# Optimization experiments

Measured on AMD Instinct MI355X. Metric: run time of the kernel, lower is better.

The kernel has to match this reference:

```python
import jax, jax.numpy as jnp
import numpy as np

# mamba-130m dims (n_layers reduced to 4 for single-device tractability)
B, L, D, DI, N, R, K, V, NL = 2, 512, 768, 1536, 16, 48, 4, 50280, 4


def setup_inputs() -> dict:
    key = jax.random.key(0)
    ks = jax.random.split(key, 10)
    s = 0.02
    return {
        "question_ids": jax.random.randint(ks[0], (B, L), 0, V, dtype=jnp.int32),
        "question_mask": jnp.ones((B, L), dtype=jnp.int32),
        "answer_ids": jax.random.randint(ks[1], (B, L), 0, V, dtype=jnp.int32),
        "answer_mask": jnp.ones((B, L), dtype=jnp.int32),
        "embed": jax.random.normal(ks[2], (V, D), jnp.float32) * s,
        "in_proj_w": jax.random.normal(ks[3], (NL, D, 2 * DI), jnp.float32) * s,
        "conv_w": jax.random.normal(ks[4], (NL, DI, K), jnp.float32) * s,
        "conv_b": jnp.zeros((NL, DI), jnp.float32),
        "x_proj_w": jax.random.normal(ks[5], (NL, DI, R + 2 * N), jnp.float32) * s,
        "dt_proj_w": jax.random.normal(ks[6], (NL, R, DI), jnp.float32) * s,
        # bias ~ -4.6 so softplus(dt) ~ 0.01, like mamba's dt init range
        "dt_proj_b": jnp.full((NL, DI), -4.6, jnp.float32),
        "A_log": jnp.broadcast_to(jnp.log(jnp.arange(1, N + 1, dtype=jnp.float32)), (NL, DI, N)) + jnp.zeros((NL, DI, N), jnp.float32),
        "D_param": jnp.ones((NL, DI), jnp.float32),
        "out_proj_w": jax.random.normal(ks[7], (NL, DI, D), jnp.float32) * s,
        "norm_w": jnp.ones((NL, D), jnp.float32),
        "norm_f_w": jnp.ones((D,), jnp.float32),
    }


def _rms(x, w, eps=1e-5):
    return x * jax.lax.rsqrt(jnp.mean(x * x, axis=-1, keepdims=True) + eps) * w


def _selective_scan(dA, dBu, Ct):
    # dA, dBu: (B, L, DI, N); Ct: (B, L, N)
    def step(h, xs):
        a, b = xs
        h = a * h + b
        return h, h

    h0 = jnp.zeros((dA.shape[0], dA.shape[2], dA.shape[3]), dA.dtype)  # (B, DI, N)
    _, hs = jax.lax.scan(step, h0, (jnp.swapaxes(dA, 0, 1), jnp.swapaxes(dBu, 0, 1)))
    hs = jnp.swapaxes(hs, 0, 1)  # (B, L, DI, N)
    return jnp.einsum('bldn,bln->bld', hs, Ct)


def _block(x, p):
    ipw, cw, cb, xpw, dtw, dtb, Alog, Dp, opw, nw = p
    h = _rms(x, nw)
    xz = h @ ipw                      # (B, L, 2*DI)
    u, z = xz[..., :DI], xz[..., DI:]
    # depthwise causal conv, kernel K
    up = jnp.pad(u, ((0, 0), (K - 1, 0), (0, 0)))
    uc = sum(up[:, k:k + u.shape[1], :] * cw[:, k] for k in range(K)) + cb
    uc = jax.nn.silu(uc)
    proj = uc @ xpw                   # (B, L, R+2N)
    dt = jax.nn.softplus(proj[..., :R] @ dtw + dtb)
    Bt = proj[..., R:R + N]
    Ct = proj[..., R + N:]
    A = -jnp.exp(Alog)                # (DI, N)
    dA = jnp.exp(dt[..., None] * A)   # (B, L, DI, N)
    dBu = (dt * uc)[..., None] * Bt[:, :, None, :]
    y = _selective_scan(dA, dBu, Ct) + uc * Dp
    y = y * jax.nn.silu(z)
    return x + y @ opw


def _lm_loss(ids, mask, embed, layers, norm_f_w):
    x = embed[ids] * mask[..., None].astype(embed.dtype)
    for p in layers:
        x = _block(x, p)
    x = _rms(x, norm_f_w)
    logits = x @ embed.T              # tied lm head, (B, L, V)
    logp = jax.nn.log_softmax(logits[:, :-1], axis=-1)
    lbl = ids[:, 1:]
    nll = -jnp.take_along_axis(logp, lbl[..., None], axis=-1)[..., 0]
    m = mask[:, 1:].astype(logp.dtype)
    return jnp.sum(nll * m) / jnp.maximum(jnp.sum(m), 1.0)


def reference(question_ids, question_mask, answer_ids, answer_mask, embed, in_proj_w, conv_w, conv_b, x_proj_w, dt_proj_w, dt_proj_b, A_log, D_param, out_proj_w, norm_w, norm_f_w):
    layers = [
        (in_proj_w[l], conv_w[l], conv_b[l], x_proj_w[l], dt_proj_w[l], dt_proj_b[l], A_log[l], D_param[l], out_proj_w[l], norm_w[l])
        for l in range(NL)
    ]
    loss_q = _lm_loss(question_ids, question_mask, embed, layers, norm_f_w)
    loss_a = _lm_loss(answer_ids, answer_mask, embed, layers, norm_f_w)
    return loss_a + loss_q
```

## Files before the change

### kernel.cpp

```cpp
#include <hip/hip_runtime.h>
#include <hip/hip_bf16.h>
#include <cstdint>
#include <cstddef>

#define T_TOK   2048
#define DM      768
#define DI      1536
#define NST     16
#define RRANK   48
#define KCONV   4
#define VOCAB   50280
#define NLAYER  4
#define SEQL    512
#define NTILE_V 393
#define NCHUNK  8
#define CHL     64

typedef __bf16 bf16x8 __attribute__((ext_vector_type(8)));
typedef float  f32x4  __attribute__((ext_vector_type(4)));

__device__ inline unsigned short f2b(float f) {
  union { float f; unsigned u; } v; v.f = f;
  unsigned r = v.u + 0x7FFFu + ((v.u >> 16) & 1u);
  return (unsigned short)(r >> 16);
}
__device__ inline float b2f(unsigned short h) {
  union { unsigned u; float f; } v; v.u = ((unsigned)h) << 16;
  return v.f;
}

__device__ inline void gload_lds16(const unsigned short* g, unsigned short* l) {
  __builtin_amdgcn_global_load_lds(
      (const __attribute__((address_space(1))) void*)g,
      (__attribute__((address_space(3))) void*)l, 16, 0, 0);
}

__global__ __launch_bounds__(256) void transpose_conv_kernel(
    const float* __restrict__ src, unsigned short* __restrict__ dst,
    int R, int C, int Rpad) {
  __shared__ float tile[32][33];
  const float* s = src + (size_t)blockIdx.z * R * C;
  unsigned short* d = dst + (size_t)blockIdx.z * C * Rpad;
  int c0 = blockIdx.x * 32, r0 = blockIdx.y * 32;
  int tx = threadIdx.x & 31, ty = threadIdx.x >> 5;
  #pragma unroll
  for (int i = 0; i < 32; i += 8) {
    int r = r0 + ty + i, c = c0 + tx;
    tile[ty + i][tx] = (r < R && c < C) ? s[(size_t)r * C + c] : 0.f;
  }
  __syncthreads();
  #pragma unroll
  for (int i = 0; i < 32; i += 8) {
    int c = c0 + ty + i, r = r0 + tx;
    if (c < C && r < Rpad) d[(size_t)c * Rpad + r] = f2b(tile[tx][ty + i]);
  }
}

__global__ __launch_bounds__(256) void cvt_embed_kernel(
    const float* __restrict__ e, unsigned short* __restrict__ eb) {
  const int n4 = VOCAB * DM / 4;
  for (int i = blockIdx.x * 256 + threadIdx.x; i < n4; i += gridDim.x * 256) {
    float4 f = *(const float4*)(e + (size_t)i * 4);
    union { unsigned long long u; unsigned short h[4]; } pk;
    pk.h[0] = f2b(f.x); pk.h[1] = f2b(f.y); pk.h[2] = f2b(f.z); pk.h[3] = f2b(f.w);
    *(unsigned long long*)(eb + (size_t)i * 4) = pk.u;
  }
}

__global__ __launch_bounds__(256) void gather_kernel(
    const int* __restrict__ qids, const int* __restrict__ qmask,
    const int* __restrict__ aids, const int* __restrict__ amask,
    const float* __restrict__ embed, float* __restrict__ x) {
  int idx = blockIdx.x * 256 + threadIdx.x;
  int t = idx / DM, d = idx - t * DM;
  int seq = t >> 9, pos = t & 511;
  const int* ids = (seq < 2) ? qids : aids;
  const int* msk = (seq < 2) ? qmask : amask;
  int s2 = seq & 1;
  int id = ids[s2 * SEQL + pos];
  float m = (float)msk[s2 * SEQL + pos];
  x[idx] = embed[(size_t)id * DM + d] * m;
}

__global__ __launch_bounds__(256) void rmsnorm_kernel(
    const float* __restrict__ x, const float* __restrict__ w,
    unsigned short* __restrict__ h) {
  int t = blockIdx.x;
  const float* xr = x + (size_t)t * DM;
  float ss = 0.f;
  for (int d = threadIdx.x; d < DM; d += 256) { float v = xr[d]; ss += v * v; }
  for (int o = 1; o < 64; o <<= 1) ss += __shfl_xor(ss, o);
  __shared__ float wsum[4];
  if ((threadIdx.x & 63) == 0) wsum[threadIdx.x >> 6] = ss;
  __syncthreads();
  ss = wsum[0] + wsum[1] + wsum[2] + wsum[3];
  float sc = rsqrtf(ss / (float)DM + 1e-5f);
  for (int d = threadIdx.x; d < DM; d += 256)
    h[(size_t)t * DM + d] = f2b(xr[d] * sc * w[d]);
}

__global__ __launch_bounds__(256) void resid_rms_kernel(
    float* __restrict__ x, const float* __restrict__ part,
    const float* __restrict__ w, unsigned short* __restrict__ h) {
  int t = blockIdx.x;
  float v[3];
  float ss = 0.f;
  #pragma unroll
  for (int j = 0; j < 3; ++j) {
    int d = threadIdx.x + j * 256;
    size_t o = (size_t)t * DM + d;
    float xv = x[o] + part[o] + part[(size_t)T_TOK * DM + o] +
               part[(size_t)2 * T_TOK * DM + o] + part[(size_t)3 * T_TOK * DM + o];
    x[o] = xv; v[j] = xv; ss += xv * xv;
  }
  for (int o = 1; o < 64; o <<= 1) ss += __shfl_xor(ss, o);
  __shared__ float wsum[4];
  if ((threadIdx.x & 63) == 0) wsum[threadIdx.x >> 6] = ss;
  __syncthreads();
  ss = wsum[0] + wsum[1] + wsum[2] + wsum[3];
  float sc = rsqrtf(ss / (float)DM + 1e-5f);
  #pragma unroll
  for (int j = 0; j < 3; ++j) {
    int d = threadIdx.x + j * 256;
    h[(size_t)t * DM + d] = f2b(v[j] * sc * w[d]);
  }
}

template <int EPI>
__global__ __launch_bounds__(256) void gemm_bf16_kernel(
    const unsigned short* __restrict__ A, int lda,
    const unsigned short* __restrict__ B, int ldb,
    float* __restrict__ C, unsigned short* __restrict__ Cbf,
    float* __restrict__ CT, int ldc,
    const float* __restrict__ bias,
    int M, int N, int K, int mtiles) {
  __shared__ __attribute__((aligned(16))) unsigned short As[2][128 * 64];
  __shared__ __attribute__((aligned(16))) unsigned short Bs[2][128 * 64];
  int bid = blockIdx.x;
  int m0 = (bid % mtiles) * 128;
  int rest = bid / mtiles;
  int n0, split = 0;
  int ntil = (N + 127) >> 7;
  if (EPI == 6) { split = rest / ntil; n0 = (rest % ntil) * 128; }
  else n0 = rest * 128;
  const unsigned short* Ap = (EPI == 6) ? A + (size_t)split * K : A;
  const unsigned short* Bp = (EPI == 6) ? B + (size_t)split * K : B;
  int tid = threadIdx.x;
  int lane = tid & 63, w = tid >> 6;
  int wr = w >> 1, wc = w & 1;
  f32x4 acc[4][4] = {};

  int lrow = lane >> 3;
  int lcol = (((lane & 7) ^ (lrow & 7)) & 7) * 8;
  auto STAGE = [&](int buf, int k0) {
    #pragma unroll
    for (int it = 0; it < 4; ++it) {
      int r = w * 32 + it * 8;
      gload_lds16(Ap + (size_t)(m0 + r + lrow) * lda + k0 + lcol, &As[buf][r * 64]);
      int br = n0 + r + lrow; if (br > N - 1) br = N - 1;
      gload_lds16(Bp + (size_t)br * ldb + k0 + lcol, &Bs[buf][r * 64]);
    }
  };

  STAGE(0, 0);
  __syncthreads();
  int nst = K / 64;
  int cur = 0;
  int rA = wr * 64 + (lane & 15);
  int rB = wc * 64 + (lane & 15);
  int sw = lane & 7, ckb = lane >> 4;
  for (int s = 0; s < nst; ++s) {
    if (s + 1 < nst) STAGE(cur ^ 1, (s + 1) * 64);
    __builtin_amdgcn_s_setprio(1);
    #pragma unroll
    for (int ks = 0; ks < 2; ++ks) {
      int ca = (((ks * 4 + ckb) ^ sw) & 7) * 8;
      bf16x8 a[4], b[4];
      #pragma unroll
      for (int i = 0; i < 4; ++i) a[i] = *(const bf16x8*)(&As[cur][(rA + i * 16) * 64 + ca]);
      #pragma unroll
      for (int i = 0; i < 4; ++i) b[i] = *(const bf16x8*)(&Bs[cur][(rB + i * 16) * 64 + ca]);
      #pragma unroll
      for (int mi = 0; mi < 4; ++mi)
        #pragma unroll
        for (int ni = 0; ni < 4; ++ni)
          acc[mi][ni] = __builtin_amdgcn_mfma_f32_16x16x32_bf16(a[mi], b[ni], acc[mi][ni], 0, 0, 0);
    }
    __builtin_amdgcn_s_setprio(0);
    __syncthreads();
    cur ^= 1;
  }

  int g = lane >> 4, c = lane & 15;
  #pragma unroll
  for (int mi = 0; mi < 4; ++mi)
    #pragma unroll
    for (int ni = 0; ni < 4; ++ni) {
      int col = n0 + wc * 64 + ni * 16 + c;
      int row0 = m0 + wr * 64 + mi * 16 + g * 4;
      if (col < N) {
        if (EPI == 5) {
          float4 o;
          float* ov = (float*)&o;
          #pragma unroll
          for (int r = 0; r < 4; ++r) {
            float xv = acc[mi][ni][r] + bias[col];
            ov[r] = (xv > 20.f) ? xv : log1pf(__expf(xv));
          }
          *(float4*)(&CT[(size_t)col * T_TOK + row0]) = o;
        } else {
          #pragma unroll
          for (int r = 0; r < 4; ++r) {
            int row = row0 + r;
            float v = acc[mi][ni][r];
            if (EPI == 0) C[(size_t)row * ldc + col] = v;
            if (EPI == 1) C[(size_t)row * ldc + col] += v;
            if (EPI == 6) C[((size_t)split * M + row) * ldc + col] = v;
          }
        }
      }
    }
}

__global__ __launch_bounds__(256) void gemm_lse_kernel(
    const unsigned short* __restrict__ A,
    const unsigned short* __restrict__ B,
    float* __restrict__ pmax, float* __restrict__ psum,
    int mtiles) {
  __shared__ __attribute__((aligned(16))) unsigned short As[2][128 * 64];
  __shared__ __attribute__((aligned(16))) unsigned short Bs[2][128 * 64];
  __shared__ float lmax[128][2];
  __shared__ float lsum[128][2];
  const int K = DM, Nv = VOCAB;
  int bid = blockIdx.x;
  int m0 = (bid % mtiles) * 128;
  int n0 = (bid / mtiles) * 128;
  int tid = threadIdx.x;
  int lane = tid & 63, w = tid >> 6;
  int wr = w >> 1, wc = w & 1;
  f32x4 acc[4][4] = {};

  int lrow = lane >> 3;
  int lcol = (((lane & 7) ^ (lrow & 7)) & 7) * 8;
  auto STAGE = [&](int buf, int k0) {
    #pragma unroll
    for (int it = 0; it < 4; ++it) {
      int r = w * 32 + it * 8;
      gload_lds16(A + (size_t)(m0 + r + lrow) * K + k0 + lcol, &As[buf][r * 64]);
      int br = n0 + r + lrow; if (br > Nv - 1) br = Nv - 1;
      gload_lds16(B + (size_t)br * K + k0 + lcol, &Bs[buf][r * 64]);
    }
  };

  STAGE(0, 0);
  __syncthreads();
  const int nst = K / 64;
  int cur = 0;
  int rA = wr * 64 + (lane & 15);
  int rB = wc * 64 + (lane & 15);
  int sw = lane & 7, ckb = lane >> 4;
  for (int s = 0; s < nst; ++s) {
    if (s + 1 < nst) STAGE(cur ^ 1, (s + 1) * 64);
    __builtin_amdgcn_s_setprio(1);
    #pragma unroll
    for (int ks = 0; ks < 2; ++ks) {
      int ca = (((ks * 4 + ckb) ^ sw) & 7) * 8;
      bf16x8 a[4], b[4];
      #pragma unroll
      for (int i = 0; i < 4; ++i) a[i] = *(const bf16x8*)(&As[cur][(rA + i * 16) * 64 + ca]);
      #pragma unroll
      for (int i = 0; i < 4; ++i) b[i] = *(const bf16x8*)(&Bs[cur][(rB + i * 16) * 64 + ca]);
      #pragma unroll
      for (int mi = 0; mi < 4; ++mi)
        #pragma unroll
        for (int ni = 0; ni < 4; ++ni)
          acc[mi][ni] = __builtin_amdgcn_mfma_f32_16x16x32_bf16(a[mi], b[ni], acc[mi][ni], 0, 0, 0);
    }
    __builtin_amdgcn_s_setprio(0);
    __syncthreads();
    cur ^= 1;
  }

  int g = lane >> 4, c = lane & 15;
  #pragma unroll
  for (int mi = 0; mi < 4; ++mi) {
    #pragma unroll
    for (int r = 0; r < 4; ++r) {
      float mx = -INFINITY;
      #pragma unroll
      for (int ni = 0; ni < 4; ++ni) {
        int col = n0 + wc * 64 + ni * 16 + c;
        float v = (col < Nv) ? acc[mi][ni][r] : -INFINITY;
        mx = fmaxf(mx, v);
      }
      mx = fmaxf(mx, __shfl_xor(mx, 1, 16));
      mx = fmaxf(mx, __shfl_xor(mx, 2, 16));
      mx = fmaxf(mx, __shfl_xor(mx, 4, 16));
      mx = fmaxf(mx, __shfl_xor(mx, 8, 16));
      float s = 0.f;
      #pragma unroll
      for (int ni = 0; ni < 4; ++ni) {
        int col = n0 + wc * 64 + ni * 16 + c;
        if (col < Nv) s += __expf(acc[mi][ni][r] - mx);
      }
      s += __shfl_xor(s, 1, 16);
      s += __shfl_xor(s, 2, 16);
      s += __shfl_xor(s, 4, 16);
      s += __shfl_xor(s, 8, 16);
      if (c == 0) {
        int rl = wr * 64 + mi * 16 + g * 4 + r;
        lmax[rl][wc] = mx;
        lsum[rl][wc] = s;
      }
    }
  }
  __syncthreads();
  if (tid < 128) {
    float m1 = lmax[tid][0], m2 = lmax[tid][1];
    float s1 = lsum[tid][0], s2 = lsum[tid][1];
    float Mx = fmaxf(m1, m2);
    float S = s1 * __expf(m1 - Mx) + s2 * __expf(m2 - Mx);
    int row = m0 + tid;
    int nb = n0 >> 7;
    pmax[(size_t)row * NTILE_V + nb] = Mx;
    psum[(size_t)row * NTILE_V + nb] = S;
  }
}

__global__ __launch_bounds__(256) void xproj_reduce_kernel(
    const float* __restrict__ part, unsigned short* __restrict__ projbf,
    float* __restrict__ BCt) {
  int idx = blockIdx.x * 256 + threadIdx.x;
  int row = idx / 80, col = idx - row * 80;
  float v = part[idx] + part[(size_t)T_TOK * 80 + idx] +
            part[(size_t)2 * T_TOK * 80 + idx] + part[(size_t)3 * T_TOK * 80 + idx];
  projbf[idx] = f2b(v);
  if (col >= RRANK) BCt[(size_t)(col - RRANK) * T_TOK + row] = v;
}

__global__ __launch_bounds__(256) void conv_silu_kernel(
    const float* __restrict__ xz, const float* __restrict__ cw,
    const float* __restrict__ cb,
    unsigned short* __restrict__ ucbf,
    float* __restrict__ ucT, float* __restrict__ zsT) {
  __shared__ float xu[67][64];
  __shared__ float ou[64][65];
  __shared__ float oz[64][65];
  int t0 = blockIdx.x * 64;
  int ch0 = blockIdx.y * 64;
  int tid = threadIdx.x;
  int cx = tid & 63, ty = tid >> 6;
  bool seq_start = (t0 & 511) == 0;
  for (int r = ty; r < 67; r += 4) {
    int tg = t0 - 3 + r;
    float v = 0.f;
    if (r >= 3 || !seq_start) v = xz[(size_t)tg * (2 * DI) + ch0 + cx];
    xu[r][cx] = v;
  }
  __syncthreads();
  int ch = ch0 + cx;
  float4 wv = *(const float4*)(cw + ch * 4);
  float bias = cb[ch];
  #pragma unroll
  for (int i = 0; i < 16; ++i) {
    int tr = ty * 16 + i;
    float a = bias + xu[tr][cx] * wv.x + xu[tr + 1][cx] * wv.y +
              xu[tr + 2][cx] * wv.z + xu[tr + 3][cx] * wv.w;
    float s = a / (1.f + __expf(-a));
    ucbf[(size_t)(t0 + tr) * DI + ch] = f2b(s);
    ou[tr][cx] = s;
    float zv = xz[(size_t)(t0 + tr) * (2 * DI) + DI + ch];
    oz[tr][cx] = zv / (1.f + __expf(-zv));
  }
  __syncthreads();
  int tx = tid & 63, cy = tid >> 6;
  #pragma unroll
  for (int i = 0; i < 16; ++i) {
    int chi = cy * 16 + i;
    ucT[(size_t)(ch0 + chi) * T_TOK + t0 + tx] = ou[tx][chi];
    zsT[(size_t)(ch0 + chi) * T_TOK + t0 + tx] = oz[tx][chi];
  }
}

__global__ __launch_bounds__(256) void scan_sum_kernel(
    const float* __restrict__ dtT, const float* __restrict__ ucT,
    const float* __restrict__ BCt, const float* __restrict__ Alog,
    float* __restrict__ Pbuf, float* __restrict__ Fbuf) {
  int bc = blockIdx.x / 96;
  int idx = (blockIdx.x % 96) * 256 + threadIdx.x;
  int n = idx & 15, d = idx >> 4;
  int b = bc >> 3, chunk = bc & 7;
  float A = -__expf(Alog[d * NST + n]);
  int t0 = b * SEQL + chunk * CHL;
  const float4* dp = (const float4*)(dtT + (size_t)d * T_TOK + t0);
  const float4* up = (const float4*)(ucT + (size_t)d * T_TOK + t0);
  const float4* Bp = (const float4*)(BCt + (size_t)n * T_TOK + t0);
  float h = 0.f, sdt = 0.f;
  #pragma unroll
  for (int q = 0; q < CHL / 4; ++q) {
    float4 d4 = dp[q], u4 = up[q], B4 = Bp[q];
    float a;
    a = __expf(d4.x * A); h = fmaf(a, h, d4.x * u4.x * B4.x);
    a = __expf(d4.y * A); h = fmaf(a, h, d4.y * u4.y * B4.y);
    a = __expf(d4.z * A); h = fmaf(a, h, d4.z * u4.z * B4.z);
    a = __expf(d4.w * A); h = fmaf(a, h, d4.w * u4.w * B4.w);
    sdt += d4.x + d4.y + d4.z + d4.w;
  }
  size_t s = ((size_t)bc * DI + d) * NST + n;
  Pbuf[s] = __expf(A * sdt);
  Fbuf[s] = h;
}

__global__ __launch_bounds__(256) void scan_emit_kernel(
    const float* __restrict__ dtT, const float* __restrict__ ucT,
    const float* __restrict__ BCt, const float* __restrict__ zsT,
    const float* __restrict__ Alog, const float* __restrict__ Dpar,
    const float* __restrict__ Pbuf, const float* __restrict__ Fbuf,
    unsigned short* __restrict__ yg) {
  int bc = blockIdx.x / 96;
  int idx = (blockIdx.x % 96) * 256 + threadIdx.x;
  int n = idx & 15, d = idx >> 4;
  int b = bc >> 3, chunk = bc & 7;
  float A = -__expf(Alog[d * NST + n]);
  float Dpv = Dpar[d];
  float h = 0.f;
  for (int j = 0; j < chunk; ++j) {
    size_t s = (((size_t)(b * NCHUNK + j)) * DI + d) * NST + n;
    h = Fbuf[s] + Pbuf[s] * h;
  }
  int t0 = b * SEQL + chunk * CHL;
  const float4* dp = (const float4*)(dtT + (size_t)d * T_TOK + t0);
  const float4* up = (const float4*)(ucT + (size_t)d * T_TOK + t0);
  const float4* Bp = (const float4*)(BCt + (size_t)n * T_TOK + t0);
  const float4* Cp = (const float4*)(BCt + (size_t)(NST + n) * T_TOK + t0);
  const float4* zp = (const float4*)(zsT + (size_t)d * T_TOK + t0);
  unsigned short* yp = yg + (size_t)t0 * DI + d;
  #pragma unroll 4
  for (int q = 0; q < CHL / 4; ++q) {
    float4 d4 = dp[q], u4 = up[q], B4 = Bp[q], C4 = Cp[q], z4 = zp[q];
    float y0, y1, y2, y3, a, cc;
    a = __expf(d4.x * A); h = fmaf(a, h, d4.x * u4.x * B4.x); cc = h * C4.x;
    cc += __shfl_xor(cc, 1, 16); cc += __shfl_xor(cc, 2, 16);
    cc += __shfl_xor(cc, 4, 16); cc += __shfl_xor(cc, 8, 16);
    y0 = (cc + u4.x * Dpv) * z4.x;
    a = __expf(d4.y * A); h = fmaf(a, h, d4.y * u4.y * B4.y); cc = h * C4.y;
    cc += __shfl_xor(cc, 1, 16); cc += __shfl_xor(cc, 2, 16);
    cc += __shfl_xor(cc, 4, 16); cc += __shfl_xor(cc, 8, 16);
    y1 = (cc + u4.y * Dpv) * z4.y;
    a = __expf(d4.z * A); h = fmaf(a, h, d4.z * u4.z * B4.z); cc = h * C4.z;
    cc += __shfl_xor(cc, 1, 16); cc += __shfl_xor(cc, 2, 16);
    cc += __shfl_xor(cc, 4, 16); cc += __shfl_xor(cc, 8, 16);
    y2 = (cc + u4.z * Dpv) * z4.z;
    a = __expf(d4.w * A); h = fmaf(a, h, d4.w * u4.w * B4.w); cc = h * C4.w;
    cc += __shfl_xor(cc, 1, 16); cc += __shfl_xor(cc, 2, 16);
    cc += __shfl_xor(cc, 4, 16); cc += __shfl_xor(cc, 8, 16);
    y3 = (cc + u4.w * Dpv) * z4.w;
    if (n == 0) {
      yp[(size_t)(q * 4 + 0) * DI] = f2b(y0);
      yp[(size_t)(q * 4 + 1) * DI] = f2b(y1);
      yp[(size_t)(q * 4 + 2) * DI] = f2b(y2);
      yp[(size_t)(q * 4 + 3) * DI] = f2b(y3);
    }
  }
}

__global__ __launch_bounds__(64) void lse_reduce_kernel(
    const float* __restrict__ pmax, const float* __restrict__ psum,
    float* __restrict__ lse) {
  int row = blockIdx.x;
  int lane = threadIdx.x;
  const float* pm = pmax + (size_t)row * NTILE_V;
  const float* ps = psum + (size_t)row * NTILE_V;
  float m = -INFINITY;
  for (int j = lane; j < NTILE_V; j += 64) m = fmaxf(m, pm[j]);
  for (int o = 1; o < 64; o <<= 1) m = fmaxf(m, __shfl_xor(m, o));
  float s = 0.f;
  for (int j = lane; j < NTILE_V; j += 64) s += ps[j] * __expf(pm[j] - m);
  for (int o = 1; o < 64; o <<= 1) s += __shfl_xor(s, o);
  if (lane == 0) lse[row] = m + __logf(s);
}

__global__ __launch_bounds__(256) void label_dot_kernel(
    const unsigned short* __restrict__ h, const unsigned short* __restrict__ eb,
    const int* __restrict__ qids, const int* __restrict__ aids,
    float* __restrict__ ldot) {
  int row = blockIdx.x * 4 + (threadIdx.x >> 6);
  int lane = threadIdx.x & 63;
  int pos = row & 511, seq = row >> 9;
  if (pos == 511) { if (lane == 0) ldot[row] = 0.f; return; }
  const int* ids = (seq < 2) ? qids : aids;
  int lbl = ids[(seq & 1) * SEQL + pos + 1];
  const unsigned short* hr = h + (size_t)row * DM;
  const unsigned short* er = eb + (size_t)lbl * DM;
  float s = 0.f;
  for (int k = lane; k < DM; k += 64) s += b2f(hr[k]) * b2f(er[k]);
  for (int o = 1; o < 64; o <<= 1) s += __shfl_xor(s, o);
  if (lane == 0) ldot[row] = s;
}

__global__ __launch_bounds__(256) void loss_kernel(
    const float* __restrict__ lse, const float* __restrict__ ldot,
    const int* __restrict__ qmask, const int* __restrict__ amask,
    float* __restrict__ out) {
  float nq = 0.f, dq = 0.f, na = 0.f, da = 0.f;
  for (int row = threadIdx.x; row < T_TOK; row += 256) {
    int pos = row & 511, seq = row >> 9;
    if (pos == 511) continue;
    const int* msk = (seq < 2) ? qmask : amask;
    float m = (float)msk[(seq & 1) * SEQL + pos + 1];
    float nll = (lse[row] - ldot[row]) * m;
    if (seq < 2) { nq += nll; dq += m; } else { na += nll; da += m; }
  }
  for (int o = 1; o < 64; o <<= 1) {
    nq += __shfl_xor(nq, o); dq += __shfl_xor(dq, o);
    na += __shfl_xor(na, o); da += __shfl_xor(da, o);
  }
  __shared__ float red[4][4];
  int w = threadIdx.x >> 6;
  if ((threadIdx.x & 63) == 0) { red[w][0] = nq; red[w][1] = dq; red[w][2] = na; red[w][3] = da; }
  __syncthreads();
  if (threadIdx.x == 0) {
    nq = 0.f; dq = 0.f; na = 0.f; da = 0.f;
    for (int i = 0; i < 4; ++i) { nq += red[i][0]; dq += red[i][1]; na += red[i][2]; da += red[i][3]; }
    float lq = nq / fmaxf(dq, 1.f);
    float la = na / fmaxf(da, 1.f);
    out[0] = lq + la;
  }
}

extern "C" void kernel_launch(void* const* d_in, const int* in_sizes, int n_in,
                              void* d_out, int out_size, void* d_ws, size_t ws_size,
                              hipStream_t stream) {
  const int*   qids  = (const int*)d_in[0];
  const int*   qmask = (const int*)d_in[1];
  const int*   aids  = (const int*)d_in[2];
  const int*   amask = (const int*)d_in[3];
  const float* embed = (const float*)d_in[4];
  const float* ipw   = (const float*)d_in[5];
  const float* cw    = (const float*)d_in[6];
  const float* cb    = (const float*)d_in[7];
  const float* xpw   = (const float*)d_in[8];
  const float* dtw   = (const float*)d_in[9];
  const float* dtb   = (const float*)d_in[10];
  const float* Alog  = (const float*)d_in[11];
  const float* Dp    = (const float*)d_in[12];
  const float* opw   = (const float*)d_in[13];
  const float* nw    = (const float*)d_in[14];
  const float* nfw   = (const float*)d_in[15];

  char* wp = (char*)d_ws;
  auto alloc = [&](size_t bytes) { char* p = wp; wp += (bytes + 255) & ~(size_t)255; return p; };

  float*          x      = (float*)alloc((size_t)T_TOK * DM * 4);
  unsigned short* hbf    = (unsigned short*)alloc((size_t)T_TOK * DM * 2);
  float*          xz     = (float*)alloc((size_t)T_TOK * 2 * DI * 4);
  unsigned short* ucbf   = (unsigned short*)alloc((size_t)T_TOK * DI * 2);
  unsigned short* projbf = (unsigned short*)alloc((size_t)T_TOK * 80 * 2);
  unsigned short* ygbf   = (unsigned short*)alloc((size_t)T_TOK * DI * 2);
  float*          ucT    = (float*)alloc((size_t)DI * T_TOK * 4);
  float*          zsT    = (float*)alloc((size_t)DI * T_TOK * 4);
  float*          dtT    = (float*)alloc((size_t)DI * T_TOK * 4);
  float*          BCt    = (float*)alloc((size_t)2 * NST * T_TOK * 4);
  float*          Pbuf   = (float*)alloc((size_t)4 * NCHUNK * DI * NST * 4);
  float*          Fbuf   = (float*)alloc((size_t)4 * NCHUNK * DI * NST * 4);
  float*          xpart  = (float*)alloc((size_t)4 * T_TOK * 80 * 4);
  unsigned short* ipw_t  = (unsigned short*)alloc((size_t)NLAYER * 2 * DI * DM * 2);
  unsigned short* opw_t  = (unsigned short*)alloc((size_t)NLAYER * DM * DI * 2);
  unsigned short* xpw_t  = (unsigned short*)alloc((size_t)NLAYER * 80 * DI * 2);
  unsigned short* dtw_t  = (unsigned short*)alloc((size_t)NLAYER * DI * 64 * 2);
  unsigned short* embbf  = (unsigned short*)alloc((size_t)VOCAB * DM * 2);
  float*          pmax   = (float*)alloc((size_t)T_TOK * NTILE_V * 4);
  float*          psum   = (float*)alloc((size_t)T_TOK * NTILE_V * 4);
  float*          lseb   = (float*)alloc((size_t)T_TOK * 4);
  float*          ldot   = (float*)alloc((size_t)T_TOK * 4);
  float*          opart  = xz;

  transpose_conv_kernel<<<dim3(96, 24, NLAYER), 256, 0, stream>>>(ipw, ipw_t, DM, 2 * DI, DM);
  transpose_conv_kernel<<<dim3(24, 48, NLAYER), 256, 0, stream>>>(opw, opw_t, DI, DM, DI);
  transpose_conv_kernel<<<dim3(3, 48, NLAYER), 256, 0, stream>>>(xpw, xpw_t, DI, 80, DI);
  transpose_conv_kernel<<<dim3(48, 2, NLAYER), 256, 0, stream>>>(dtw, dtw_t, RRANK, DI, 64);
  cvt_embed_kernel<<<2048, 256, 0, stream>>>(embed, embbf);

  gather_kernel<<<(T_TOK * DM) / 256, 256, 0, stream>>>(qids, qmask, aids, amask, embed, x);
  rmsnorm_kernel<<<T_TOK, 256, 0, stream>>>(x, nw, hbf);

  const int mt = T_TOK / 128;
  for (int l = 0; l < NLAYER; ++l) {
    gemm_bf16_kernel<0><<<mt * (2 * DI / 128), 256, 0, stream>>>(
        hbf, DM, ipw_t + (size_t)l * 2 * DI * DM, DM, xz, nullptr, nullptr, 2 * DI,
        nullptr, T_TOK, 2 * DI, DM, mt);
    conv_silu_kernel<<<dim3(T_TOK / 64, DI / 64), 256, 0, stream>>>(
        xz, cw + (size_t)l * DI * KCONV, cb + (size_t)l * DI, ucbf, ucT, zsT);
    gemm_bf16_kernel<6><<<mt * 1 * 4, 256, 0, stream>>>(
        ucbf, DI, xpw_t + (size_t)l * 80 * DI, DI, xpart, nullptr, nullptr, 80,
        nullptr, T_TOK, 80, DI / 4, mt);
    xproj_reduce_kernel<<<(T_TOK * 80) / 256, 256, 0, stream>>>(xpart, projbf, BCt);
    gemm_bf16_kernel<5><<<mt * (DI / 128), 256, 0, stream>>>(
        projbf, 80, dtw_t + (size_t)l * DI * 64, 64, nullptr, nullptr, dtT, DI,
        dtb + (size_t)l * DI, T_TOK, DI, 64, mt);
    scan_sum_kernel<<<32 * 96, 256, 0, stream>>>(
        dtT, ucT, BCt, Alog + (size_t)l * DI * NST, Pbuf, Fbuf);
    scan_emit_kernel<<<32 * 96, 256, 0, stream>>>(
        dtT, ucT, BCt, zsT, Alog + (size_t)l * DI * NST, Dp + (size_t)l * DI,
        Pbuf, Fbuf, ygbf);
    gemm_bf16_kernel<6><<<mt * (DM / 128) * 4, 256, 0, stream>>>(
        ygbf, DI, opw_t + (size_t)l * DM * DI, DI, opart, nullptr, nullptr, DM,
        nullptr, T_TOK, DM, DI / 4, mt);
    resid_rms_kernel<<<T_TOK, 256, 0, stream>>>(
        x, opart, (l < NLAYER - 1) ? (nw + (l + 1) * DM) : nfw, hbf);
  }

  gemm_lse_kernel<<<mt * NTILE_V, 256, 0, stream>>>(hbf, embbf, pmax, psum, mt);
  lse_reduce_kernel<<<T_TOK, 64, 0, stream>>>(pmax, psum, lseb);
  label_dot_kernel<<<T_TOK / 4, 256, 0, stream>>>(hbf, embbf, qids, aids, ldot);
  loss_kernel<<<1, 256, 0, stream>>>(lseb, ldot, qmask, amask, (float*)d_out);
}
```

Baseline: 1.161 ms.

## Fuse z-gate SiLU into in_proj GEMM epilogue and swizzle LSE GEMM block order

```diff
diff --git a/kernel.cpp b/kernel.cpp
--- a/kernel.cpp
+++ b/kernel.cpp
@@ -208,6 +208,21 @@
             ov[r] = (xv > 20.f) ? xv : log1pf(__expf(xv));
           }
           *(float4*)(&CT[(size_t)col * T_TOK + row0]) = o;
+        } else if (EPI == 7) {
+          if (col < DI) {
+            #pragma unroll
+            for (int r = 0; r < 4; ++r)
+              C[(size_t)(row0 + r) * DI + col] = acc[mi][ni][r];
+          } else {
+            float4 o;
+            float* ov = (float*)&o;
+            #pragma unroll
+            for (int r = 0; r < 4; ++r) {
+              float zv = acc[mi][ni][r];
+              ov[r] = zv / (1.f + __expf(-zv));
+            }
+            *(float4*)(&CT[(size_t)(col - DI) * T_TOK + row0]) = o;
+          }
         } else {
           #pragma unroll
           for (int r = 0; r < 4; ++r) {
@@ -233,6 +248,8 @@
   __shared__ float lsum[128][2];
   const int K = DM, Nv = VOCAB;
   int bid = blockIdx.x;
+  int cpx = gridDim.x >> 3;
+  bid = (bid & 7) * cpx + (bid >> 3);
   int m0 = (bid % mtiles) * 128;
   int n0 = (bid / mtiles) * 128;
   int tid = threadIdx.x;
@@ -339,13 +356,11 @@
 }
 
 __global__ __launch_bounds__(256) void conv_silu_kernel(
-    const float* __restrict__ xz, const float* __restrict__ cw,
+    const float* __restrict__ ur, const float* __restrict__ cw,
     const float* __restrict__ cb,
-    unsigned short* __restrict__ ucbf,
-    float* __restrict__ ucT, float* __restrict__ zsT) {
+    unsigned short* __restrict__ ucbf, float* __restrict__ ucT) {
   __shared__ float xu[67][64];
   __shared__ float ou[64][65];
-  __shared__ float oz[64][65];
   int t0 = blockIdx.x * 64;
   int ch0 = blockIdx.y * 64;
   int tid = threadIdx.x;
@@ -354,7 +369,7 @@
   for (int r = ty; r < 67; r += 4) {
     int tg = t0 - 3 + r;
     float v = 0.f;
-    if (r >= 3 || !seq_start) v = xz[(size_t)tg * (2 * DI) + ch0 + cx];
+    if (r >= 3 || !seq_start) v = ur[(size_t)tg * DI + ch0 + cx];
     xu[r][cx] = v;
   }
   __syncthreads();
@@ -369,8 +384,6 @@
     float s = a / (1.f + __expf(-a));
     ucbf[(size_t)(t0 + tr) * DI + ch] = f2b(s);
     ou[tr][cx] = s;
-    float zv = xz[(size_t)(t0 + tr) * (2 * DI) + DI + ch];
-    oz[tr][cx] = zv / (1.f + __expf(-zv));
   }
   __syncthreads();
   int tx = tid & 63, cy = tid >> 6;
@@ -378,7 +391,6 @@
   for (int i = 0; i < 16; ++i) {
     int chi = cy * 16 + i;
     ucT[(size_t)(ch0 + chi) * T_TOK + t0 + tx] = ou[tx][chi];
-    zsT[(size_t)(ch0 + chi) * T_TOK + t0 + tx] = oz[tx][chi];
   }
 }
 
@@ -553,7 +565,7 @@
 
   float*          x      = (float*)alloc((size_t)T_TOK * DM * 4);
   unsigned short* hbf    = (unsigned short*)alloc((size_t)T_TOK * DM * 2);
-  float*          xz     = (float*)alloc((size_t)T_TOK * 2 * DI * 4);
+  float*          ur     = (float*)alloc((size_t)T_TOK * DI * 4);
   unsigned short* ucbf   = (unsigned short*)alloc((size_t)T_TOK * DI * 2);
   unsigned short* projbf = (unsigned short*)alloc((size_t)T_TOK * 80 * 2);
   unsigned short* ygbf   = (unsigned short*)alloc((size_t)T_TOK * DI * 2);
@@ -564,6 +576,7 @@
   float*          Pbuf   = (float*)alloc((size_t)4 * NCHUNK * DI * NST * 4);
   float*          Fbuf   = (float*)alloc((size_t)4 * NCHUNK * DI * NST * 4);
   float*          xpart  = (float*)alloc((size_t)4 * T_TOK * 80 * 4);
+  float*          opart  = (float*)alloc((size_t)4 * T_TOK * DM * 4);
   unsigned short* ipw_t  = (unsigned short*)alloc((size_t)NLAYER * 2 * DI * DM * 2);
   unsigned short* opw_t  = (unsigned short*)alloc((size_t)NLAYER * DM * DI * 2);
   unsigned short* xpw_t  = (unsigned short*)alloc((size_t)NLAYER * 80 * DI * 2);
@@ -573,7 +586,6 @@
   float*          psum   = (float*)alloc((size_t)T_TOK * NTILE_V * 4);
   float*          lseb   = (float*)alloc((size_t)T_TOK * 4);
   float*          ldot   = (float*)alloc((size_t)T_TOK * 4);
-  float*          opart  = xz;
 
   transpose_conv_kernel<<<dim3(96, 24, NLAYER), 256, 0, stream>>>(ipw, ipw_t, DM, 2 * DI, DM);
   transpose_conv_kernel<<<dim3(24, 48, NLAYER), 256, 0, stream>>>(opw, opw_t, DI, DM, DI);
@@ -586,11 +598,11 @@
 
   const int mt = T_TOK / 128;
   for (int l = 0; l < NLAYER; ++l) {
-    gemm_bf16_kernel<0><<<mt * (2 * DI / 128), 256, 0, stream>>>(
-        hbf, DM, ipw_t + (size_t)l * 2 * DI * DM, DM, xz, nullptr, nullptr, 2 * DI,
+    gemm_bf16_kernel<7><<<mt * (2 * DI / 128), 256, 0, stream>>>(
+        hbf, DM, ipw_t + (size_t)l * 2 * DI * DM, DM, ur, nullptr, zsT, DI,
         nullptr, T_TOK, 2 * DI, DM, mt);
     conv_silu_kernel<<<dim3(T_TOK / 64, DI / 64), 256, 0, stream>>>(
-        xz, cw + (size_t)l * DI * KCONV, cb + (size_t)l * DI, ucbf, ucT, zsT);
+        ur, cw + (size_t)l * DI * KCONV, cb + (size_t)l * DI, ucbf, ucT);
     gemm_bf16_kernel<6><<<mt * 1 * 4, 256, 0, stream>>>(
         ucbf, DI, xpw_t + (size_t)l * 80 * DI, DI, xpart, nullptr, nullptr, 80,
         nullptr, T_TOK, 80, DI / 4, mt);
```

Result: slower. 1.191 ms (+2.6%).
